# Kernel tuning notes

Measured on AMD Instinct MI355X. Metric: run time of the kernel, lower is better.

## Reference

```python
import jax, jax.numpy as jnp
import numpy as np

N = 512      # nodes
E = 16384    # edges (avg degree 32)
D = 128      # indim
OUT = 128    # outdim


def setup_inputs() -> dict:
    key = jax.random.key(0)
    k1, k2, k3 = jax.random.split(key, 3)
    X = jax.random.normal(k1, (N, N, D), dtype=jnp.float32)
    edge_index = jax.random.randint(k2, (2, E), 0, N, dtype=jnp.int64)
    W = jax.random.normal(k3, (3 * D, OUT), dtype=jnp.float32) * (1.0 / np.sqrt(3 * D))
    b = jnp.zeros((OUT,), dtype=jnp.float32)
    return {"X": X, "edge_index": edge_index, "W": W, "b": b}


def reference(X, edge_index, W, b):
    # X: [N, N, D] tuple features X[i, j] for (subgraph root i, node j)
    # edge_index: [2, E] directed edges (src -> dst), aggr = 'sum'
    n = X.shape[0]
    src, dst = edge_index[0], edge_index[1]
    # Dense binary adjacency (sum aggregation counts multi-edges, matching
    # scatter-add over the edge list). A[k, j] = #edges k -> j.
    A = jnp.zeros((n, n), dtype=X.dtype).at[src, dst].add(jnp.ones((src.shape[0],), X.dtype))
    # OpMessagePassingOnSubg2D: within subgraph i, aggregate over neighbors of j
    # X1[i, j] = sum_{k in N(j)} X[i, k]
    X1 = jnp.einsum('kj,ikd->ijd', A, X)
    # OpMessagePassingCrossSubg2D: across subgraphs, aggregate over neighbors of i
    # X2[i, j] = sum_{k in N(i)} X[k, j]
    X2 = jnp.einsum('ki,kjd->ijd', A, X)
    # catvalue([X1, X2]) -> [X, X1, X2], then pointwise MLP (single Linear)
    H = jnp.concatenate([X, X1, X2], axis=-1)  # [N, N, 3D]
    return H @ W + b  # [N, N, OUT]
```

## Files before the change

### kernel.cpp

```cpp
#include <hip/hip_runtime.h>
#include <hip/hip_bf16.h>
#include <stdint.h>

#define NN 512
#define DD 128
#define EE 16384
#define K3 384

typedef short bf16x8 __attribute__((ext_vector_type(8)));
typedef short bf16x4 __attribute__((ext_vector_type(4)));
typedef float f32x4  __attribute__((ext_vector_type(4)));
typedef unsigned int u32;

__device__ __forceinline__ short f2bf(float f) {
    union { __hip_bfloat16 h; short s; } u;
    u.h = __float2bfloat16(f);
    return u.s;
}
__device__ __forceinline__ u32 pk2(float a, float b) {
    return (u32)(unsigned short)f2bf(a) | ((u32)(unsigned short)f2bf(b) << 16);
}

typedef __attribute__((address_space(3))) unsigned int lds_u32;
typedef __attribute__((address_space(1))) const unsigned int glb_u32;
__device__ __forceinline__ void gll16(void* l, const void* g) {
    __builtin_amdgcn_global_load_lds((glb_u32*)g, (lds_u32*)l, 16, 0, 0);
}


__global__ void k_zero(float* __restrict__ At) {
    At[blockIdx.x * 256 + threadIdx.x] = 0.0f;
}

__global__ void k_edges(const int* __restrict__ ei, float* __restrict__ At) {
    __shared__ int flag;
    if (threadIdx.x == 0) flag = 0;
    __syncthreads();
    int any = 0;
    for (int i = threadIdx.x; i < EE; i += blockDim.x) any |= ei[2 * i + 1];
    if (any) atomicOr(&flag, 1);
    __syncthreads();
    const bool is32 = (flag != 0);
    for (int e = threadIdx.x; e < EE; e += blockDim.x) {
        int src, dst;
        if (is32) { src = ei[e];     dst = ei[EE + e]; }
        else      { src = ei[2 * e]; dst = ei[2 * (EE + e)]; }
        atomicAdd(&At[dst * NN + src], 1.0f);
    }
}

__global__ void k_cast_at(const float* __restrict__ At, short* __restrict__ Atb) {
    int t = blockIdx.x * 256 + threadIdx.x;
    Atb[t] = f2bf(At[t]);
}

__global__ void k_wt2(const float* __restrict__ W, short* __restrict__ Wt2) {
    int t = blockIdx.x * 256 + threadIdx.x;
    int kk = t >> 7, n = t & 127;
    int s = kk >> 7, d = kk & 127;
    Wt2[s * 16384 + n * 128 + d] = f2bf(W[t]);
}

__global__ __launch_bounds__(256) void k_y(const float* __restrict__ X,
                                           const short* __restrict__ Wt2,
                                           short* __restrict__ Y1T,
                                           short* __restrict__ Y2) {
    __shared__ __align__(16) short Xs[16384];
    __shared__ __align__(16) short Ws[16384];

    const int tid  = threadIdx.x;
    const int lane = tid & 63;
    const int wv   = tid >> 6;
    const int wr   = (wv >> 1) * 64;
    const int wc   = (wv & 1) * 64;
    const int lm   = lane & 15;
    const int lq   = lane >> 4;
    const int i  = blockIdx.x >> 2;
    const int j0 = (blockIdx.x & 3) * 128;

    #pragma unroll
    for (int it = 0; it < 16; ++it) {
        int g = tid + it * 256;
        int r = g >> 5, c4 = g & 31;
        float4 v = *(const float4*)&X[i * 65536 + (j0 + r) * 128 + c4 * 4];
        int kb = c4 >> 4, c = c4 & 15, p = c >> 1, h2 = c & 1;
        bf16x4 pc; pc[0] = f2bf(v.x); pc[1] = f2bf(v.y); pc[2] = f2bf(v.z); pc[3] = f2bf(v.w);
        *(bf16x4*)&Xs[kb * 8192 + r * 64 + ((p ^ (r & 7)) * 8 + h2 * 4)] = pc;
    }

    #pragma unroll
    for (int s = 1; s <= 2; ++s) {
        #pragma unroll
        for (int it = 0; it < 8; ++it) {
            int slot = it * 256 + tid;
            int kb = slot >> 10, rem = slot & 1023;
            int n = rem >> 3, pc = rem & 7;
            gll16(&Ws[slot * 8],
                  &Wt2[s * 16384 + n * 128 + kb * 64 + ((pc ^ (n & 7)) * 8)]);
        }
        __syncthreads();

        f32x4 acc[4][4] = {};
        #pragma unroll
        for (int kb = 0; kb < 2; ++kb)
            #pragma unroll
            for (int ks = 0; ks < 2; ++ks) {
                bf16x8 af[4], bf[4];
                #pragma unroll
                for (int mf = 0; mf < 4; ++mf) {
                    int R = wr + mf * 16 + lm, Cc = ks * 4 + lq;
                    af[mf] = *(const bf16x8*)&Xs[kb * 8192 + R * 64 + (Cc ^ (R & 7)) * 8];
                }
                #pragma unroll
                for (int nf = 0; nf < 4; ++nf) {
                    int R = wc + nf * 16 + lm, Cc = ks * 4 + lq;
                    bf[nf] = *(const bf16x8*)&Ws[kb * 8192 + R * 64 + (Cc ^ (R & 7)) * 8];
                }
                #pragma unroll
                for (int mf = 0; mf < 4; ++mf)
                    #pragma unroll
                    for (int nf = 0; nf < 4; ++nf)
                        acc[mf][nf] = __builtin_amdgcn_mfma_f32_16x16x32_bf16(
                            af[mf], bf[nf], acc[mf][nf], 0, 0, 0);
            }
        __syncthreads();

        if (s == 1) {
            u32* T = (u32*)Ws;
            #pragma unroll
            for (int mf = 0; mf < 4; ++mf)
                #pragma unroll
                for (int nf = 0; nf < 4; ++nf) {
                    int n = wc + nf * 16 + lm;
                    int jb = wr + mf * 16 + lq * 4;
                    int w = jb >> 1;
                    u32 lo = pk2(acc[mf][nf][0], acc[mf][nf][1]);
                    u32 hi = pk2(acc[mf][nf][2], acc[mf][nf][3]);
                    uint2 val; val.x = lo; val.y = hi;
                    *(uint2*)&T[n * 64 + (w ^ (n & 28))] = val;
                }
            __syncthreads();
            #pragma unroll
            for (int it = 0; it < 8; ++it) {
                int ch = tid & 15, n = (tid >> 4) + it * 16;
                uint4 q = *(const uint4*)&T[n * 64 + ((ch * 4) ^ (n & 28))];
                *(uint4*)&Y1T[i * 65536 + n * 512 + j0 + ch * 8] = q;
            }
            __syncthreads();
        } else {
            #pragma unroll
            for (int mf = 0; mf < 4; ++mf)
                #pragma unroll
                for (int nf = 0; nf < 4; ++nf)
                    #pragma unroll
                    for (int r = 0; r < 4; ++r)
                        Ws[(wr + mf * 16 + lq * 4 + r) * 128 + wc + nf * 16 + lm]
                            = f2bf(acc[mf][nf][r]);
            __syncthreads();
            #pragma unroll
            for (int it = 0; it < 8; ++it) {
                int q = tid + it * 256;
                int row = q >> 4, oc = (q & 15) * 8;
                *(bf16x8*)&Y2[i * 65536 + (j0 + row) * 128 + oc]
                    = *(const bf16x8*)&Ws[row * 128 + oc];
            }
        }
    }
}

__global__ __launch_bounds__(256) void k_t(const short* __restrict__ Y2,
                                           short* __restrict__ Y2T) {
    __shared__ __align__(16) u32 U[128 * 64];
    const int tid = threadIdx.x;
    const int j  = blockIdx.x >> 2;
    const int k0 = (blockIdx.x & 3) * 128;

    const int c8 = tid & 15;
    const int a0 = tid >> 4;
    #pragma unroll
    for (int it = 0; it < 4; ++it) {
        int a = a0 + it * 16;
        const short* r0 = &Y2[(size_t)(k0 + 2 * a) * 65536 + j * 128 + c8 * 8];
        bf16x8 A0 = *(const bf16x8*)r0;
        bf16x8 A1 = *(const bf16x8*)(r0 + 65536);
        #pragma unroll
        for (int cc = 0; cc < 8; ++cc) {
            int n = c8 * 8 + cc;
            U[n * 64 + (a ^ (n & 28))] =
                (u32)(unsigned short)A0[cc] | ((u32)(unsigned short)A1[cc] << 16);
        }
    }
    __syncthreads();
    const int ch = tid & 15;
    const int n0 = tid >> 4;
    #pragma unroll
    for (int it = 0; it < 8; ++it) {
        int n = n0 + it * 16;
        uint4 q = *(const uint4*)&U[n * 64 + ((ch * 4) ^ (n & 28))];
        *(uint4*)&Y2T[j * 65536 + n * 512 + k0 + ch * 8] = q;
    }
}

__global__ __launch_bounds__(256) void k_a1(const short* __restrict__ Atb,
                                            const short* __restrict__ Y1T,
                                            short* __restrict__ P1) {
    __shared__ __align__(16) short sm[16384];
    short* As = sm;
    short* Bs = sm + 8192;

    const int tid  = threadIdx.x;
    const int lane = tid & 63;
    const int wv   = tid >> 6;
    const int wr   = (wv >> 1) * 64;
    const int wc   = (wv & 1) * 64;
    const int lm   = lane & 15;
    const int lq   = lane >> 4;
    const int i  = blockIdx.x >> 2;
    const int a0 = (blockIdx.x & 3) * 128;

    f32x4 acc[4][4] = {};

    for (int kb = 0; kb < 8; ++kb) {
        const int k0 = kb * 64;
        #pragma unroll
        for (int it = 0; it < 4; ++it) {
            int slot = it * 256 + tid;
            int r = slot >> 3, p = slot & 7;
            int cg = (p ^ (r & 7)) * 8;
            gll16(&As[slot * 8], &Atb[(a0 + r) * 512 + k0 + cg]);
            gll16(&Bs[slot * 8], &Y1T[i * 65536 + r * 512 + k0 + cg]);
        }
        __syncthreads();
        #pragma unroll
        for (int ks = 0; ks < 2; ++ks) {
            bf16x8 af[4], bf[4];
            #pragma unroll
            for (int mf = 0; mf < 4; ++mf) {
                int R = wr + mf * 16 + lm, Cc = ks * 4 + lq;
                af[mf] = *(const bf16x8*)&As[R * 64 + (Cc ^ (R & 7)) * 8];
            }
            #pragma unroll
            for (int nf = 0; nf < 4; ++nf) {
                int R = wc + nf * 16 + lm, Cc = ks * 4 + lq;
                bf[nf] = *(const bf16x8*)&Bs[R * 64 + (Cc ^ (R & 7)) * 8];
            }
            #pragma unroll
            for (int mf = 0; mf < 4; ++mf)
                #pragma unroll
                for (int nf = 0; nf < 4; ++nf)
                    acc[mf][nf] = __builtin_amdgcn_mfma_f32_16x16x32_bf16(
                        af[mf], bf[nf], acc[mf][nf], 0, 0, 0);
        }
        __syncthreads();
    }

    #pragma unroll
    for (int mf = 0; mf < 4; ++mf)
        #pragma unroll
        for (int nf = 0; nf < 4; ++nf)
            #pragma unroll
            for (int r = 0; r < 4; ++r)
                sm[(wr + mf * 16 + lq * 4 + r) * 128 + wc + nf * 16 + lm]
                    = f2bf(acc[mf][nf][r]);
    __syncthreads();
    #pragma unroll
    for (int it = 0; it < 8; ++it) {
        int q = tid + it * 256;
        int row = q >> 4, oc = (q & 15) * 8;
        *(bf16x8*)&P1[i * 65536 + (a0 + row) * 128 + oc]
            = *(const bf16x8*)&sm[row * 128 + oc];
    }
}

__global__ __launch_bounds__(256) void k_a2f(const float* __restrict__ X,
                                             const short* __restrict__ Atb,
                                             const short* __restrict__ Y2T,
                                             const short* __restrict__ Wt2,
                                             const short* __restrict__ P1,
                                             const float* __restrict__ bias,
                                             float* __restrict__ out) {
    __shared__ __align__(16) short sm[16384];
    short* As = sm;
    short* Bs = sm + 8192;

    const int tid  = threadIdx.x;
    const int lane = tid & 63;
    const int wv   = tid >> 6;
    const int wr   = (wv >> 1) * 64;
    const int wc   = (wv & 1) * 64;
    const int lm   = lane & 15;
    const int lq   = lane >> 4;
    const int j  = blockIdx.x >> 2;
    const int i0 = (blockIdx.x & 3) * 128;

    f32x4 acc[4][4] = {};

    #pragma unroll
    for (int kb = 0; kb < 2; ++kb) {
        #pragma unroll
        for (int it = 0; it < 8; ++it) {
            int g = tid + it * 256;
            int r = g >> 4, c4 = g & 15;
            float4 v = *(const float4*)&X[(size_t)(i0 + r) * 65536 + j * 128 + kb * 64 + c4 * 4];
            int p = c4 >> 1, h2 = c4 & 1;
            bf16x4 pc; pc[0] = f2bf(v.x); pc[1] = f2bf(v.y); pc[2] = f2bf(v.z); pc[3] = f2bf(v.w);
            *(bf16x4*)&As[r * 64 + ((p ^ (r & 7)) * 8 + h2 * 4)] = pc;
        }
        #pragma unroll
        for (int it = 0; it < 4; ++it) {
            int slot = it * 256 + tid;
            int n = slot >> 3, pc = slot & 7;
            gll16(&Bs[slot * 8], &Wt2[n * 128 + kb * 64 + ((pc ^ (n & 7)) * 8)]);
        }
        __syncthreads();
        #pragma unroll
        for (int ks = 0; ks < 2; ++ks) {
            bf16x8 af[4], bf[4];
            #pragma unroll
            for (int mf = 0; mf < 4; ++mf) {
                int R = wr + mf * 16 + lm, Cc = ks * 4 + lq;
                af[mf] = *(const bf16x8*)&As[R * 64 + (Cc ^ (R & 7)) * 8];
            }
            #pragma unroll
            for (int nf = 0; nf < 4; ++nf) {
                int R = wc + nf * 16 + lm, Cc = ks * 4 + lq;
                bf[nf] = *(const bf16x8*)&Bs[R * 64 + (Cc ^ (R & 7)) * 8];
            }
            #pragma unroll
            for (int mf = 0; mf < 4; ++mf)
                #pragma unroll
                for (int nf = 0; nf < 4; ++nf)
                    acc[mf][nf] = __builtin_amdgcn_mfma_f32_16x16x32_bf16(
                        af[mf], bf[nf], acc[mf][nf], 0, 0, 0);
        }
        __syncthreads();
    }

    for (int kb = 0; kb < 8; ++kb) {
        const int k0 = kb * 64;
        #pragma unroll
        for (int it = 0; it < 4; ++it) {
            int slot = it * 256 + tid;
            int r = slot >> 3, p = slot & 7;
            int cg = (p ^ (r & 7)) * 8;
            gll16(&As[slot * 8], &Atb[(i0 + r) * 512 + k0 + cg]);
            gll16(&Bs[slot * 8], &Y2T[j * 65536 + r * 512 + k0 + cg]);
        }
        __syncthreads();
        #pragma unroll
        for (int ks = 0; ks < 2; ++ks) {
            bf16x8 af[4], bf[4];
            #pragma unroll
            for (int mf = 0; mf < 4; ++mf) {
                int R = wr + mf * 16 + lm, Cc = ks * 4 + lq;
                af[mf] = *(const bf16x8*)&As[R * 64 + (Cc ^ (R & 7)) * 8];
            }
            #pragma unroll
            for (int nf = 0; nf < 4; ++nf) {
                int R = wc + nf * 16 + lm, Cc = ks * 4 + lq;
                bf[nf] = *(const bf16x8*)&Bs[R * 64 + (Cc ^ (R & 7)) * 8];
            }
            #pragma unroll
            for (int mf = 0; mf < 4; ++mf)
                #pragma unroll
                for (int nf = 0; nf < 4; ++nf)
                    acc[mf][nf] = __builtin_amdgcn_mfma_f32_16x16x32_bf16(
                        af[mf], bf[nf], acc[mf][nf], 0, 0, 0);
        }
        __syncthreads();
    }

    #pragma unroll
    for (int mf = 0; mf < 4; ++mf)
        #pragma unroll
        for (int nf = 0; nf < 4; ++nf)
            #pragma unroll
            for (int r = 0; r < 4; ++r)
                sm[(wr + mf * 16 + lq * 4 + r) * 128 + wc + nf * 16 + lm]
                    = f2bf(acc[mf][nf][r]);
    __syncthreads();
    #pragma unroll
    for (int it = 0; it < 8; ++it) {
        int q = tid + it * 256;
        int row = q >> 4, oc = (q & 15) * 8;
        bf16x8 vs = *(const bf16x8*)&sm[row * 128 + oc];
        bf16x8 vp = *(const bf16x8*)&P1[(size_t)(i0 + row) * 65536 / 512 * 512 + 0];
        (void)vp;
        const short* p1p = &P1[(size_t)(i0 + row) * 65536 + j * 128 + oc];
        bf16x8 vpl = *(const bf16x8*)p1p;
        float4 b0 = *(const float4*)&bias[oc];
        float4 b1 = *(const float4*)&bias[oc + 4];
        union { short s; __hip_bfloat16 h; } cs, cp;
        float o[8];
        #pragma unroll
        for (int e = 0; e < 8; ++e) {
            cs.s = vs[e]; cp.s = vpl[e];
            o[e] = __bfloat162float(cs.h) + __bfloat162float(cp.h);
        }
        o[0] += b0.x; o[1] += b0.y; o[2] += b0.z; o[3] += b0.w;
        o[4] += b1.x; o[5] += b1.y; o[6] += b1.z; o[7] += b1.w;
        float* op = &out[(size_t)(i0 + row) * 65536 + j * 128 + oc];
        float4 w0; w0.x = o[0]; w0.y = o[1]; w0.z = o[2]; w0.w = o[3];
        float4 w1; w1.x = o[4]; w1.y = o[5]; w1.z = o[6]; w1.w = o[7];
        *(float4*)op = w0;
        *(float4*)(op + 4) = w1;
    }
}


__global__ __launch_bounds__(256) void k_agg_fb(const float* __restrict__ X,
                                                const float* __restrict__ At,
                                                short* __restrict__ X1b,
                                                short* __restrict__ X2b) {
    __shared__ short As[128 * 72];
    __shared__ short Bs[128 * 72];
    const int tid  = threadIdx.x;
    const int lane = tid & 63;
    const int wv   = tid >> 6;
    const int wr   = (wv >> 1) * 64;
    const int wc   = (wv & 1) * 64;
    const int lm   = lane & 15;
    const int lq   = lane >> 4;
    int a0, Bbase, Bks, Cbase, Crs;
    short* Cp;
    const int bidx = blockIdx.x;
    if (bidx < 2048) {
        int i = bidx >> 2, jt = bidx & 3;
        a0 = jt * 128; Bbase = i * 65536; Bks = 128;
        Cbase = i * 65536 + jt * 16384; Crs = 128; Cp = X1b;
    } else {
        int bb = bidx - 2048;
        int j = bb >> 2, it = bb & 3;
        a0 = it * 128; Bbase = j * 128; Bks = 65536;
        Cbase = it * 8388608 + j * 128; Crs = 65536; Cp = X2b;
    }
    f32x4 acc[4][4] = {};
    const int d  = tid & 127;
    const int kh = tid >> 7;
    for (int kb = 0; kb < 8; ++kb) {
        const int k0 = kb * 64;
        #pragma unroll
        for (int it8 = 0; it8 < 8; ++it8) {
            int g = tid + it8 * 256;
            int r = g >> 4, kq = (g & 15) * 4;
            float4 v = *(const float4*)&At[(a0 + r) * 512 + k0 + kq];
            bf16x4 p; p[0] = f2bf(v.x); p[1] = f2bf(v.y); p[2] = f2bf(v.z); p[3] = f2bf(v.w);
            *(bf16x4*)&As[r * 72 + kq] = p;
        }
        #pragma unroll
        for (int gi = 0; gi < 4; ++gi) {
            int kg = kh * 4 + gi;
            bf16x8 p;
            #pragma unroll
            for (int jj = 0; jj < 8; ++jj)
                p[jj] = f2bf(X[Bbase + (k0 + kg * 8 + jj) * Bks + d]);
            *(bf16x8*)&Bs[d * 72 + kg * 8] = p;
        }
        __syncthreads();
        #pragma unroll
        for (int ks = 0; ks < 2; ++ks) {
            bf16x8 af[4], bfr[4];
            #pragma unroll
            for (int mf = 0; mf < 4; ++mf)
                af[mf] = *(const bf16x8*)&As[(wr + mf * 16 + lm) * 72 + ks * 32 + lq * 8];
            #pragma unroll
            for (int nf = 0; nf < 4; ++nf)
                bfr[nf] = *(const bf16x8*)&Bs[(wc + nf * 16 + lm) * 72 + ks * 32 + lq * 8];
            #pragma unroll
            for (int mf = 0; mf < 4; ++mf)
                #pragma unroll
                for (int nf = 0; nf < 4; ++nf)
                    acc[mf][nf] = __builtin_amdgcn_mfma_f32_16x16x32_bf16(
                        af[mf], bfr[nf], acc[mf][nf], 0, 0, 0);
        }
        __syncthreads();
    }
    #pragma unroll
    for (int mf = 0; mf < 4; ++mf)
        #pragma unroll
        for (int nf = 0; nf < 4; ++nf)
            #pragma unroll
            for (int r = 0; r < 4; ++r) {
                int row = wr + mf * 16 + lq * 4 + r;
                int col = wc + nf * 16 + lm;
                Cp[Cbase + row * Crs + col] = f2bf(acc[mf][nf][r]);
            }
}

__global__ __launch_bounds__(256) void k_final_fb(const float* __restrict__ X,
                                                  const short* __restrict__ X1b,
                                                  const short* __restrict__ X2b,
                                                  const short* __restrict__ Wt2,
                                                  const float* __restrict__ bias,
                                                  float* __restrict__ out) {
    __shared__ short As[128 * 72];
    __shared__ short Ws[128 * 72];
    const int tid  = threadIdx.x;
    const int lane = tid & 63;
    const int wv   = tid >> 6;
    const int wr   = (wv >> 1) * 64;
    const int wc   = (wv & 1) * 64;
    const int lm   = lane & 15;
    const int lq   = lane >> 4;
    const int m0   = blockIdx.x * 128;
    f32x4 acc[4][4] = {};
    for (int ph = 0; ph < 6; ++ph) {
        const int s = ph >> 1, h = ph & 1;
        if (s == 0) {
            #pragma unroll
            for (int it8 = 0; it8 < 8; ++it8) {
                int g = tid + it8 * 256;
                int r = g >> 4, kq = (g & 15) * 4;
                float4 v = *(const float4*)&X[(m0 + r) * 128 + h * 64 + kq];
                bf16x4 p; p[0] = f2bf(v.x); p[1] = f2bf(v.y); p[2] = f2bf(v.z); p[3] = f2bf(v.w);
                *(bf16x4*)&As[r * 72 + kq] = p;
            }
        } else {
            const short* src = (s == 1) ? X1b : X2b;
            #pragma unroll
            for (int it4 = 0; it4 < 4; ++it4) {
                int g = tid + it4 * 256;
                int r = g >> 3, ko = (g & 7) * 8;
                *(bf16x8*)&As[r * 72 + ko] =
                    *(const bf16x8*)&src[(m0 + r) * 128 + h * 64 + ko];
            }
        }
        #pragma unroll
        for (int it4 = 0; it4 < 4; ++it4) {
            int g = tid + it4 * 256;
            int n = g >> 3, ko = (g & 7) * 8;
            *(bf16x8*)&Ws[n * 72 + ko] =
                *(const bf16x8*)&Wt2[s * 16384 + n * 128 + h * 64 + ko];
        }
        __syncthreads();
        #pragma unroll
        for (int ks = 0; ks < 2; ++ks) {
            bf16x8 af[4], bfr[4];
            #pragma unroll
            for (int mf = 0; mf < 4; ++mf)
                af[mf] = *(const bf16x8*)&As[(wr + mf * 16 + lm) * 72 + ks * 32 + lq * 8];
            #pragma unroll
            for (int nf = 0; nf < 4; ++nf)
                bfr[nf] = *(const bf16x8*)&Ws[(wc + nf * 16 + lm) * 72 + ks * 32 + lq * 8];
            #pragma unroll
            for (int mf = 0; mf < 4; ++mf)
                #pragma unroll
                for (int nf = 0; nf < 4; ++nf)
                    acc[mf][nf] = __builtin_amdgcn_mfma_f32_16x16x32_bf16(
                        af[mf], bfr[nf], acc[mf][nf], 0, 0, 0);
        }
        __syncthreads();
    }
    #pragma unroll
    for (int nf = 0; nf < 4; ++nf) {
        float bv = bias[wc + nf * 16 + lm];
        #pragma unroll
        for (int mf = 0; mf < 4; ++mf)
            #pragma unroll
            for (int r = 0; r < 4; ++r) {
                int row = m0 + wr + mf * 16 + lq * 4 + r;
                int col = wc + nf * 16 + lm;
                out[row * 128 + col] = acc[mf][nf][r] + bv;
            }
    }
}

extern "C" void kernel_launch(void* const* d_in, const int* in_sizes, int n_in,
                              void* d_out, int out_size, void* d_ws, size_t ws_size,
                              hipStream_t stream) {
    const float* X  = (const float*)d_in[0];
    const int*   ei = (const int*)d_in[1];
    const float* W  = (const float*)d_in[2];
    const float* b  = (const float*)d_in[3];
    float* out = (float*)d_out;
    char* ws = (char*)d_ws;
    const size_t MB = 1u << 20;

    float* At  = (float*)ws;
    short* Atb = (short*)(ws + 1 * MB);
    short* Wt2 = (short*)(ws + 1 * MB + 512 * 1024);

    k_zero   <<<1024, 256, 0, stream>>>(At);
    k_edges  <<<1, 1024, 0, stream>>>(ei, At);
    k_wt2    <<<192, 256, 0, stream>>>(W, Wt2);
    k_cast_at<<<1024, 256, 0, stream>>>(At, Atb);

    if (ws_size >= 194 * MB) {
        short* Y1T = (short*)(ws + 2 * MB);
        short* Y2  = (short*)(ws + 66 * MB);
        short* Y2T = (short*)(ws + 130 * MB);
        short* P1  = Y2;
        k_y  <<<2048, 256, 0, stream>>>(X, Wt2, Y1T, Y2);
        k_t  <<<2048, 256, 0, stream>>>(Y2, Y2T);
        k_a1 <<<2048, 256, 0, stream>>>(Atb, Y1T, P1);
        k_a2f<<<2048, 256, 0, stream>>>(X, Atb, Y2T, Wt2, P1, b, out);
    } else {
        short* X1b = (short*)(ws + 2 * MB);
        short* X2b = (short*)(ws + 66 * MB);
        k_agg_fb  <<<4096, 256, 0, stream>>>(X, At, X1b, X2b);
        k_final_fb<<<2048, 256, 0, stream>>>(X, X1b, X2b, Wt2, b, out);
    }
}
```

Before: 475.4 us.

## Fuse Y projection and within-subgraph aggregation into one per-slab kernel

Replaces the separate k_y and k_a1 kernels with k_slab. Each k_slab block handles one subgraph row i. It projects X through both weight slices, keeps the Y1 chunk in shared memory and immediately multiplies it by the adjacency, so the Y1T intermediate never goes through global memory. The adjacency is pre-packed into an MFMA-fragment layout (k_pack_at), letting both k_slab and k_a2f read A fragments straight from global memory instead of staging them in LDS. The trade-offs are 128KB of LDS per 512-thread block, uncoalesced scalar Y2 stores, and only 512 blocks.

```diff
diff --git a/kernel.cpp b/kernel.cpp
--- a/kernel.cpp
+++ b/kernel.cpp
@@ -5,7 +5,6 @@
 #define NN 512
 #define DD 128
 #define EE 16384
-#define K3 384
 
 typedef short bf16x8 __attribute__((ext_vector_type(8)));
 typedef short bf16x4 __attribute__((ext_vector_type(4)));
@@ -49,11 +48,6 @@
     }
 }
 
-__global__ void k_cast_at(const float* __restrict__ At, short* __restrict__ Atb) {
-    int t = blockIdx.x * 256 + threadIdx.x;
-    Atb[t] = f2bf(At[t]);
-}
-
 __global__ void k_wt2(const float* __restrict__ W, short* __restrict__ Wt2) {
     int t = blockIdx.x * 256 + threadIdx.x;
     int kk = t >> 7, n = t & 127;
@@ -61,110 +55,152 @@
     Wt2[s * 16384 + n * 128 + d] = f2bf(W[t]);
 }
 
-__global__ __launch_bounds__(256) void k_y(const float* __restrict__ X,
-                                           const short* __restrict__ Wt2,
-                                           short* __restrict__ Y1T,
-                                           short* __restrict__ Y2) {
-    __shared__ __align__(16) short Xs[16384];
-    __shared__ __align__(16) short Ws[16384];
+__global__ void k_pack_at(const float* __restrict__ At, short* __restrict__ Atp) {
+    int t = blockIdx.x * 256 + threadIdx.x;
+    int T = t >> 6, l = t & 63;
+    int row = (T >> 4) * 16 + (l & 15);
+    int col = (T & 15) * 32 + (l >> 4) * 8;
+    const float* s = &At[row * 512 + col];
+    bf16x8 p;
+    #pragma unroll
+    for (int e = 0; e < 8; ++e) p[e] = f2bf(s[e]);
+    *(bf16x8*)&Atp[(size_t)T * 512 + l * 8] = p;
+}
+
+__global__ __launch_bounds__(512, 2) void k_slab(const float* __restrict__ X,
+                                                 const short* __restrict__ Wt2,
+                                                 const short* __restrict__ Atp,
+                                                 short* __restrict__ Y2,
+                                                 short* __restrict__ Pp) {
+    __shared__ __align__(16) short sh[65536];
+    short* Xc = sh;
+    short* Yc = sh + 16384;
+    short* Lw = sh + 32768;
 
     const int tid  = threadIdx.x;
     const int lane = tid & 63;
     const int wv   = tid >> 6;
-    const int wr   = (wv >> 1) * 64;
-    const int wc   = (wv & 1) * 64;
     const int lm   = lane & 15;
     const int lq   = lane >> 4;
-    const int i  = blockIdx.x >> 2;
-    const int j0 = (blockIdx.x & 3) * 128;
-
-    #pragma unroll
-    for (int it = 0; it < 16; ++it) {
-        int g = tid + it * 256;
-        int r = g >> 5, c4 = g & 31;
-        float4 v = *(const float4*)&X[i * 65536 + (j0 + r) * 128 + c4 * 4];
-        int kb = c4 >> 4, c = c4 & 15, p = c >> 1, h2 = c & 1;
-        bf16x4 pc; pc[0] = f2bf(v.x); pc[1] = f2bf(v.y); pc[2] = f2bf(v.z); pc[3] = f2bf(v.w);
-        *(bf16x4*)&Xs[kb * 8192 + r * 64 + ((p ^ (r & 7)) * 8 + h2 * 4)] = pc;
-    }
-
-    #pragma unroll
-    for (int s = 1; s <= 2; ++s) {
+    const int i    = blockIdx.x;
+
+    const int mw   = wv & 1;
+    const int quad = wv >> 1;
+    const int rowh = quad & 1;
+    const int colh = quad >> 1;
+    const int wr   = wv * 64;
+
+    #pragma unroll
+    for (int it = 0; it < 8; ++it) {
+        int slot = it * 512 + tid;
+        int s01 = slot >> 11, kb = (slot >> 10) & 1;
+        int n = (slot >> 3) & 127, pc = slot & 7;
+        gll16(&Lw[slot * 8],
+              &Wt2[(1 + s01) * 16384 + n * 128 + kb * 64 + ((pc ^ (n & 7)) * 8)]);
+    }
+
+    f32x4 acc[4][8] = {};
+
+    for (int kc = 0; kc < 4; ++kc) {
+        if (kc) __syncthreads();
         #pragma unroll
         for (int it = 0; it < 8; ++it) {
-            int slot = it * 256 + tid;
-            int kb = slot >> 10, rem = slot & 1023;
-            int n = rem >> 3, pc = rem & 7;
-            gll16(&Ws[slot * 8],
-                  &Wt2[s * 16384 + n * 128 + kb * 64 + ((pc ^ (n & 7)) * 8)]);
-        }
-        __syncthreads();
-
-        f32x4 acc[4][4] = {};
-        #pragma unroll
-        for (int kb = 0; kb < 2; ++kb)
+            int g = tid + it * 512;
+            int r = g >> 5, c4 = g & 31;
+            float4 v = *(const float4*)&X[(size_t)i * 65536 + (kc * 128 + r) * 128 + c4 * 4];
+            int kb = c4 >> 4, c = c4 & 15, p = c >> 1, h2 = c & 1;
+            bf16x4 pcv; pcv[0] = f2bf(v.x); pcv[1] = f2bf(v.y); pcv[2] = f2bf(v.z); pcv[3] = f2bf(v.w);
+            *(bf16x4*)&Xc[kb * 8192 + r * 64 + ((p ^ (r & 7)) * 8 + h2 * 4)] = pcv;
+        }
+        __syncthreads();
+
+        f32x4 ay[4][4] = {};
+        #pragma unroll
+        for (int sl = 0; sl < 4; ++sl) {
+            int kb = sl >> 1, ks = sl & 1, Cc = ks * 4 + lq;
+            bf16x8 af[4], bw[4];
+            #pragma unroll
+            for (int mf = 0; mf < 4; ++mf) {
+                int R = rowh * 64 + mf * 16 + lm;
+                af[mf] = *(const bf16x8*)&Xc[kb * 8192 + R * 64 + ((Cc ^ (R & 7)) * 8)];
+            }
+            #pragma unroll
+            for (int nf = 0; nf < 4; ++nf) {
+                int R = colh * 64 + nf * 16 + lm;
+                bw[nf] = *(const bf16x8*)&Lw[mw * 16384 + kb * 8192 + R * 64 + ((Cc ^ (R & 7)) * 8)];
+            }
+            #pragma unroll
+            for (int mf = 0; mf < 4; ++mf)
+                #pragma unroll
+                for (int nf = 0; nf < 4; ++nf)
+                    ay[mf][nf] = __builtin_amdgcn_mfma_f32_16x16x32_bf16(
+                        af[mf], bw[nf], ay[mf][nf], 0, 0, 0);
+        }
+        if (mw == 0) {
+            #pragma unroll
+            for (int mf = 0; mf < 4; ++mf)
+                #pragma unroll
+                for (int nf = 0; nf < 4; ++nf)
+                    #pragma unroll
+                    for (int rr = 0; rr < 4; ++rr) {
+                        int rl64 = mf * 16 + lq * 4 + rr;
+                        int n = colh * 64 + nf * 16 + lm;
+                        Yc[rowh * 8192 + n * 64 + (((rl64 >> 3) ^ (n & 7)) * 8 + (rl64 & 7))]
+                            = f2bf(ay[mf][nf][rr]);
+                    }
+        } else {
+            #pragma unroll
+            for (int mf = 0; mf < 4; ++mf)
+                #pragma unroll
+                for (int nf = 0; nf < 4; ++nf)
+                    #pragma unroll
+                    for (int rr = 0; rr < 4; ++rr) {
+                        int row = kc * 128 + rowh * 64 + mf * 16 + lq * 4 + rr;
+                        int n = colh * 64 + nf * 16 + lm;
+                        Y2[(size_t)i * 65536 + row * 128 + n] = f2bf(ay[mf][nf][rr]);
+                    }
+        }
+        __syncthreads();
+
+        #pragma unroll
+        for (int kb2 = 0; kb2 < 2; ++kb2)
             #pragma unroll
             for (int ks = 0; ks < 2; ++ks) {
-                bf16x8 af[4], bf[4];
-                #pragma unroll
-                for (int mf = 0; mf < 4; ++mf) {
-                    int R = wr + mf * 16 + lm, Cc = ks * 4 + lq;
-                    af[mf] = *(const bf16x8*)&Xs[kb * 8192 + R * 64 + (Cc ^ (R & 7)) * 8];
-                }
-                #pragma unroll
-                for (int nf = 0; nf < 4; ++nf) {
-                    int R = wc + nf * 16 + lm, Cc = ks * 4 + lq;
-                    bf[nf] = *(const bf16x8*)&Ws[kb * 8192 + R * 64 + (Cc ^ (R & 7)) * 8];
+                int kt = kc * 4 + kb2 * 2 + ks;
+                bf16x8 af[4], bf[8];
+                #pragma unroll
+                for (int mf = 0; mf < 4; ++mf)
+                    af[mf] = *(const bf16x8*)&Atp[(size_t)((wv * 4 + mf) * 16 + kt) * 512 + lane * 8];
+                #pragma unroll
+                for (int nf = 0; nf < 8; ++nf) {
+                    int R = nf * 16 + lm;
+                    bf[nf] = *(const bf16x8*)&Yc[kb2 * 8192 + R * 64 + (((ks * 4 + lq) ^ (R & 7)) * 8)];
                 }
                 #pragma unroll
                 for (int mf = 0; mf < 4; ++mf)
                     #pragma unroll
-                    for (int nf = 0; nf < 4; ++nf)
+                    for (int nf = 0; nf < 8; ++nf)
                         acc[mf][nf] = __builtin_amdgcn_mfma_f32_16x16x32_bf16(
                             af[mf], bf[nf], acc[mf][nf], 0, 0, 0);
             }
-        __syncthreads();
-
-        if (s == 1) {
-            u32* T = (u32*)Ws;
-            #pragma unroll
-            for (int mf = 0; mf < 4; ++mf)
-                #pragma unroll
-                for (int nf = 0; nf < 4; ++nf) {
-                    int n = wc + nf * 16 + lm;
-                    int jb = wr + mf * 16 + lq * 4;
-                    int w = jb >> 1;
-                    u32 lo = pk2(acc[mf][nf][0], acc[mf][nf][1]);
-                    u32 hi = pk2(acc[mf][nf][2], acc[mf][nf][3]);
-                    uint2 val; val.x = lo; val.y = hi;
-                    *(uint2*)&T[n * 64 + (w ^ (n & 28))] = val;
-                }
-            __syncthreads();
-            #pragma unroll
-            for (int it = 0; it < 8; ++it) {
-                int ch = tid & 15, n = (tid >> 4) + it * 16;
-                uint4 q = *(const uint4*)&T[n * 64 + ((ch * 4) ^ (n & 28))];
-                *(uint4*)&Y1T[i * 65536 + n * 512 + j0 + ch * 8] = q;
-            }
-            __syncthreads();
-        } else {
-            #pragma unroll
-            for (int mf = 0; mf < 4; ++mf)
-                #pragma unroll
-                for (int nf = 0; nf < 4; ++nf)
-                    #pragma unroll
-                    for (int r = 0; r < 4; ++r)
-                        Ws[(wr + mf * 16 + lq * 4 + r) * 128 + wc + nf * 16 + lm]
-                            = f2bf(acc[mf][nf][r]);
-            __syncthreads();
-            #pragma unroll
-            for (int it = 0; it < 8; ++it) {
-                int q = tid + it * 256;
-                int row = q >> 4, oc = (q & 15) * 8;
-                *(bf16x8*)&Y2[i * 65536 + (j0 + row) * 128 + oc]
-                    = *(const bf16x8*)&Ws[row * 128 + oc];
-            }
-        }
+    }
+    __syncthreads();
+
+    #pragma unroll
+    for (int mf = 0; mf < 4; ++mf)
+        #pragma unroll
+        for (int nf = 0; nf < 8; ++nf)
+            #pragma unroll
+            for (int rr = 0; rr < 4; ++rr)
+                sh[(wr + mf * 16 + lq * 4 + rr) * 128 + nf * 16 + lm]
+                    = f2bf(acc[mf][nf][rr]);
+    __syncthreads();
+    #pragma unroll
+    for (int it = 0; it < 16; ++it) {
+        int q = tid + it * 512;
+        int row = q >> 4, oc = (q & 15) * 8;
+        *(bf16x8*)&Pp[(size_t)i * 65536 + row * 128 + oc]
+            = *(const bf16x8*)&sh[row * 128 + oc];
     }
 }
 
@@ -201,82 +237,11 @@
     }
 }
 
-__global__ __launch_bounds__(256) void k_a1(const short* __restrict__ Atb,
-                                            const short* __restrict__ Y1T,
-                                            short* __restrict__ P1) {
-    __shared__ __align__(16) short sm[16384];
-    short* As = sm;
-    short* Bs = sm + 8192;
-
-    const int tid  = threadIdx.x;
-    const int lane = tid & 63;
-    const int wv   = tid >> 6;
-    const int wr   = (wv >> 1) * 64;
-    const int wc   = (wv & 1) * 64;
-    const int lm   = lane & 15;
-    const int lq   = lane >> 4;
-    const int i  = blockIdx.x >> 2;
-    const int a0 = (blockIdx.x & 3) * 128;
-
-    f32x4 acc[4][4] = {};
-
-    for (int kb = 0; kb < 8; ++kb) {
-        const int k0 = kb * 64;
-        #pragma unroll
-        for (int it = 0; it < 4; ++it) {
-            int slot = it * 256 + tid;
-            int r = slot >> 3, p = slot & 7;
-            int cg = (p ^ (r & 7)) * 8;
-            gll16(&As[slot * 8], &Atb[(a0 + r) * 512 + k0 + cg]);
-            gll16(&Bs[slot * 8], &Y1T[i * 65536 + r * 512 + k0 + cg]);
-        }
-        __syncthreads();
-        #pragma unroll
-        for (int ks = 0; ks < 2; ++ks) {
-            bf16x8 af[4], bf[4];
-            #pragma unroll
-            for (int mf = 0; mf < 4; ++mf) {
-                int R = wr + mf * 16 + lm, Cc = ks * 4 + lq;
-                af[mf] = *(const bf16x8*)&As[R * 64 + (Cc ^ (R & 7)) * 8];
-            }
-            #pragma unroll
-            for (int nf = 0; nf < 4; ++nf) {
-                int R = wc + nf * 16 + lm, Cc = ks * 4 + lq;
-                bf[nf] = *(const bf16x8*)&Bs[R * 64 + (Cc ^ (R & 7)) * 8];
-            }
-            #pragma unroll
-            for (int mf = 0; mf < 4; ++mf)
-                #pragma unroll
-                for (int nf = 0; nf < 4; ++nf)
-                    acc[mf][nf] = __builtin_amdgcn_mfma_f32_16x16x32_bf16(
-                        af[mf], bf[nf], acc[mf][nf], 0, 0, 0);
-        }
-        __syncthreads();
-    }
-
-    #pragma unroll
-    for (int mf = 0; mf < 4; ++mf)
-        #pragma unroll
-        for (int nf = 0; nf < 4; ++nf)
-            #pragma unroll
-            for (int r = 0; r < 4; ++r)
-                sm[(wr + mf * 16 + lq * 4 + r) * 128 + wc + nf * 16 + lm]
-                    = f2bf(acc[mf][nf][r]);
-    __syncthreads();
-    #pragma unroll
-    for (int it = 0; it < 8; ++it) {
-        int q = tid + it * 256;
-        int row = q >> 4, oc = (q & 15) * 8;
-        *(bf16x8*)&P1[i * 65536 + (a0 + row) * 128 + oc]
-            = *(const bf16x8*)&sm[row * 128 + oc];
-    }
-}
-
 __global__ __launch_bounds__(256) void k_a2f(const float* __restrict__ X,
-                                             const short* __restrict__ Atb,
+                                             const short* __restrict__ Atp,
                                              const short* __restrict__ Y2T,
                                              const short* __restrict__ Wt2,
-                                             const short* __restrict__ P1,
+                                             const short* __restrict__ Pp,
                                              const float* __restrict__ bias,
                                              float* __restrict__ out) {
     __shared__ __align__(16) short sm[16384];
@@ -336,6 +301,7 @@
         __syncthreads();
     }
 
+    const int jt0 = (i0 >> 4) + (wr >> 4);
     for (int kb = 0; kb < 8; ++kb) {
         const int k0 = kb * 64;
         #pragma unroll
@@ -343,18 +309,16 @@
             int slot = it * 256 + tid;
             int r = slot >> 3, p = slot & 7;
             int cg = (p ^ (r & 7)) * 8;
-            gll16(&As[slot * 8], &Atb[(i0 + r) * 512 + k0 + cg]);
             gll16(&Bs[slot * 8], &Y2T[j * 65536 + r * 512 + k0 + cg]);
         }
         __syncthreads();
         #pragma unroll
         for (int ks = 0; ks < 2; ++ks) {
+            int kt = kb * 2 + ks;
             bf16x8 af[4], bf[4];
             #pragma unroll
-            for (int mf = 0; mf < 4; ++mf) {
-                int R = wr + mf * 16 + lm, Cc = ks * 4 + lq;
-                af[mf] = *(const bf16x8*)&As[R * 64 + (Cc ^ (R & 7)) * 8];
-            }
+            for (int mf = 0; mf < 4; ++mf)
+                af[mf] = *(const bf16x8*)&Atp[(size_t)((jt0 + mf) * 16 + kt) * 512 + lane * 8];
             #pragma unroll
             for (int nf = 0; nf < 4; ++nf) {
                 int R = wc + nf * 16 + lm, Cc = ks * 4 + lq;
@@ -384,10 +348,7 @@
         int q = tid + it * 256;
         int row = q >> 4, oc = (q & 15) * 8;
         bf16x8 vs = *(const bf16x8*)&sm[row * 128 + oc];
-        bf16x8 vp = *(const bf16x8*)&P1[(size_t)(i0 + row) * 65536 / 512 * 512 + 0];
-        (void)vp;
-        const short* p1p = &P1[(size_t)(i0 + row) * 65536 + j * 128 + oc];
-        bf16x8 vpl = *(const bf16x8*)p1p;
+        bf16x8 vpl = *(const bf16x8*)&Pp[(size_t)(i0 + row) * 65536 + j * 128 + oc];
         float4 b0 = *(const float4*)&bias[oc];
         float4 b1 = *(const float4*)&bias[oc + 4];
         union { short s; __hip_bfloat16 h; } cs, cp;
@@ -577,23 +538,21 @@
     const size_t MB = 1u << 20;
 
     float* At  = (float*)ws;
-    short* Atb = (short*)(ws + 1 * MB);
+    short* Atp = (short*)(ws + 1 * MB);
     short* Wt2 = (short*)(ws + 1 * MB + 512 * 1024);
 
     k_zero   <<<1024, 256, 0, stream>>>(At);
     k_edges  <<<1, 1024, 0, stream>>>(ei, At);
     k_wt2    <<<192, 256, 0, stream>>>(W, Wt2);
-    k_cast_at<<<1024, 256, 0, stream>>>(At, Atb);
+    k_pack_at<<<128, 256, 0, stream>>>(At, Atp);
 
     if (ws_size >= 194 * MB) {
-        short* Y1T = (short*)(ws + 2 * MB);
-        short* Y2  = (short*)(ws + 66 * MB);
-        short* Y2T = (short*)(ws + 130 * MB);
-        short* P1  = Y2;
-        k_y  <<<2048, 256, 0, stream>>>(X, Wt2, Y1T, Y2);
-        k_t  <<<2048, 256, 0, stream>>>(Y2, Y2T);
-        k_a1 <<<2048, 256, 0, stream>>>(Atb, Y1T, P1);
-        k_a2f<<<2048, 256, 0, stream>>>(X, Atb, Y2T, Wt2, P1, b, out);
+        short* Y2  = (short*)(ws + 2 * MB);
+        short* Y2T = (short*)(ws + 66 * MB);
+        short* Pp  = (short*)(ws + 130 * MB);
+        k_slab<<<512, 512, 0, stream>>>(X, Wt2, Atp, Y2, Pp);
+        k_t   <<<2048, 256, 0, stream>>>(Y2, Y2T);
+        k_a2f <<<2048, 256, 0, stream>>>(X, Atp, Y2T, Wt2, Pp, b, out);
     } else {
         short* X1b = (short*)(ws + 2 * MB);
         short* X2b = (short*)(ws + 66 * MB);
```

Result: slower. 524.5 us (+10.3%).

## Pre-pack adjacency into MFMA fragment layout, double-buffer B tiles, swizzle block order

Applied to the files above, without the earlier changes.

The bf16 adjacency matrix is now packed once into a per-lane MFMA fragment layout. The aggregation GEMMs can then read A fragments straight from global/L2 instead of staging them through LDS. The freed LDS is used to double-buffer the Y1T/Y2T tiles, so the next tile's load overlaps the current MFMAs. Block indices in k_t, k_a1 and k_a2f are remapped with a stride-8 swizzle, likely to spread consecutive blocks across XCDs for better L2 locality. The risks are A-fragment latency from global memory and a possible race, because the loop no longer has a barrier before the next tile overwrites its buffer.

```diff
diff --git a/kernel.cpp b/kernel.cpp
--- a/kernel.cpp
+++ b/kernel.cpp
@@ -5,7 +5,6 @@
 #define NN 512
 #define DD 128
 #define EE 16384
-#define K3 384
 
 typedef short bf16x8 __attribute__((ext_vector_type(8)));
 typedef short bf16x4 __attribute__((ext_vector_type(4)));
@@ -49,16 +48,23 @@
     }
 }
 
-__global__ void k_cast_at(const float* __restrict__ At, short* __restrict__ Atb) {
-    int t = blockIdx.x * 256 + threadIdx.x;
-    Atb[t] = f2bf(At[t]);
-}
-
 __global__ void k_wt2(const float* __restrict__ W, short* __restrict__ Wt2) {
     int t = blockIdx.x * 256 + threadIdx.x;
     int kk = t >> 7, n = t & 127;
     int s = kk >> 7, d = kk & 127;
     Wt2[s * 16384 + n * 128 + d] = f2bf(W[t]);
+}
+
+__global__ void k_pack_at(const float* __restrict__ At, short* __restrict__ Atp) {
+    int t = blockIdx.x * 256 + threadIdx.x;
+    int T = t >> 6, l = t & 63;
+    int row = (T >> 4) * 16 + (l & 15);
+    int col = (T & 15) * 32 + (l >> 4) * 8;
+    const float* s = &At[row * 512 + col];
+    bf16x8 p;
+    #pragma unroll
+    for (int e = 0; e < 8; ++e) p[e] = f2bf(s[e]);
+    *(bf16x8*)&Atp[(size_t)T * 512 + l * 8] = p;
 }
 
 __global__ __launch_bounds__(256) void k_y(const float* __restrict__ X,
@@ -172,8 +178,9 @@
                                            short* __restrict__ Y2T) {
     __shared__ __align__(16) u32 U[128 * 64];
     const int tid = threadIdx.x;
-    const int j  = blockIdx.x >> 2;
-    const int k0 = (blockIdx.x & 3) * 128;
+    const int bid = (blockIdx.x & 7) * 256 + (blockIdx.x >> 3);
+    const int j  = bid >> 2;
+    const int k0 = (bid & 3) * 128;
 
     const int c8 = tid & 15;
     const int a0 = tid >> 4;
@@ -201,12 +208,10 @@
     }
 }
 
-__global__ __launch_bounds__(256) void k_a1(const short* __restrict__ Atb,
+__global__ __launch_bounds__(256) void k_a1(const short* __restrict__ Atp,
                                             const short* __restrict__ Y1T,
                                             short* __restrict__ P1) {
     __shared__ __align__(16) short sm[16384];
-    short* As = sm;
-    short* Bs = sm + 8192;
 
     const int tid  = threadIdx.x;
     const int lane = tid & 63;
@@ -215,34 +220,46 @@
     const int wc   = (wv & 1) * 64;
     const int lm   = lane & 15;
     const int lq   = lane >> 4;
-    const int i  = blockIdx.x >> 2;
-    const int a0 = (blockIdx.x & 3) * 128;
+    const int bid = (blockIdx.x & 7) * 256 + (blockIdx.x >> 3);
+    const int i  = bid >> 2;
+    const int a0 = (bid & 3) * 128;
+    const int jt0 = (a0 >> 4) + (wr >> 4);
 
     f32x4 acc[4][4] = {};
 
+    #pragma unroll
+    for (int it = 0; it < 4; ++it) {
+        int slot = it * 256 + tid;
+        int r = slot >> 3, p = slot & 7;
+        int cg = (p ^ (r & 7)) * 8;
+        gll16(&sm[slot * 8], &Y1T[i * 65536 + r * 512 + cg]);
+    }
+    __syncthreads();
+
     for (int kb = 0; kb < 8; ++kb) {
-        const int k0 = kb * 64;
-        #pragma unroll
-        for (int it = 0; it < 4; ++it) {
-            int slot = it * 256 + tid;
-            int r = slot >> 3, p = slot & 7;
-            int cg = (p ^ (r & 7)) * 8;
-            gll16(&As[slot * 8], &Atb[(a0 + r) * 512 + k0 + cg]);
-            gll16(&Bs[slot * 8], &Y1T[i * 65536 + r * 512 + k0 + cg]);
-        }
-        __syncthreads();
+        short* cur = (kb & 1) ? sm + 8192 : sm;
+        short* nxt = (kb & 1) ? sm : sm + 8192;
+        if (kb < 7) {
+            const int k0n = (kb + 1) * 64;
+            #pragma unroll
+            for (int it = 0; it < 4; ++it) {
+                int slot = it * 256 + tid;
+                int r = slot >> 3, p = slot & 7;
+                int cg = (p ^ (r & 7)) * 8;
+                gll16(&nxt[slot * 8], &Y1T[i * 65536 + r * 512 + k0n + cg]);
+            }
+        }
         #pragma unroll
         for (int ks = 0; ks < 2; ++ks) {
+            int kt = kb * 2 + ks;
             bf16x8 af[4], bf[4];
             #pragma unroll
-            for (int mf = 0; mf < 4; ++mf) {
-                int R = wr + mf * 16 + lm, Cc = ks * 4 + lq;
-                af[mf] = *(const bf16x8*)&As[R * 64 + (Cc ^ (R & 7)) * 8];
-            }
+            for (int mf = 0; mf < 4; ++mf)
+                af[mf] = *(const bf16x8*)&Atp[(size_t)((jt0 + mf) * 16 + kt) * 512 + lane * 8];
             #pragma unroll
             for (int nf = 0; nf < 4; ++nf) {
                 int R = wc + nf * 16 + lm, Cc = ks * 4 + lq;
-                bf[nf] = *(const bf16x8*)&Bs[R * 64 + (Cc ^ (R & 7)) * 8];
+                bf[nf] = *(const bf16x8*)&cur[R * 64 + (Cc ^ (R & 7)) * 8];
             }
             #pragma unroll
             for (int mf = 0; mf < 4; ++mf)
@@ -273,7 +290,7 @@
 }
 
 __global__ __launch_bounds__(256) void k_a2f(const float* __restrict__ X,
-                                             const short* __restrict__ Atb,
+                                             const short* __restrict__ Atp,
                                              const short* __restrict__ Y2T,
                                              const short* __restrict__ Wt2,
                                              const short* __restrict__ P1,
@@ -290,8 +307,9 @@
     const int wc   = (wv & 1) * 64;
     const int lm   = lane & 15;
     const int lq   = lane >> 4;
-    const int j  = blockIdx.x >> 2;
-    const int i0 = (blockIdx.x & 3) * 128;
+    const int bid = (blockIdx.x & 7) * 256 + (blockIdx.x >> 3);
+    const int j  = bid >> 2;
+    const int i0 = (bid & 3) * 128;
 
     f32x4 acc[4][4] = {};
 
@@ -336,29 +354,40 @@
         __syncthreads();
     }
 
+    const int jt0 = (i0 >> 4) + (wr >> 4);
+    #pragma unroll
+    for (int it = 0; it < 4; ++it) {
+        int slot = it * 256 + tid;
+        int r = slot >> 3, p = slot & 7;
+        int cg = (p ^ (r & 7)) * 8;
+        gll16(&sm[slot * 8], &Y2T[j * 65536 + r * 512 + cg]);
+    }
+    __syncthreads();
+
     for (int kb = 0; kb < 8; ++kb) {
-        const int k0 = kb * 64;
-        #pragma unroll
-        for (int it = 0; it < 4; ++it) {
-            int slot = it * 256 + tid;
-            int r = slot >> 3, p = slot & 7;
-            int cg = (p ^ (r & 7)) * 8;
-            gll16(&As[slot * 8], &Atb[(i0 + r) * 512 + k0 + cg]);
-            gll16(&Bs[slot * 8], &Y2T[j * 65536 + r * 512 + k0 + cg]);
-        }
-        __syncthreads();
+        short* cur = (kb & 1) ? sm + 8192 : sm;
+        short* nxt = (kb & 1) ? sm : sm + 8192;
+        if (kb < 7) {
+            const int k0n = (kb + 1) * 64;
+            #pragma unroll
+            for (int it = 0; it < 4; ++it) {
+                int slot = it * 256 + tid;
+                int r = slot >> 3, p = slot & 7;
+                int cg = (p ^ (r & 7)) * 8;
+                gll16(&nxt[slot * 8], &Y2T[j * 65536 + r * 512 + k0n + cg]);
+            }
+        }
         #pragma unroll
         for (int ks = 0; ks < 2; ++ks) {
+            int kt = kb * 2 + ks;
             bf16x8 af[4], bf[4];
             #pragma unroll
-            for (int mf = 0; mf < 4; ++mf) {
-                int R = wr + mf * 16 + lm, Cc = ks * 4 + lq;
-                af[mf] = *(const bf16x8*)&As[R * 64 + (Cc ^ (R & 7)) * 8];
-            }
+            for (int mf = 0; mf < 4; ++mf)
+                af[mf] = *(const bf16x8*)&Atp[(size_t)((jt0 + mf) * 16 + kt) * 512 + lane * 8];
             #pragma unroll
             for (int nf = 0; nf < 4; ++nf) {
                 int R = wc + nf * 16 + lm, Cc = ks * 4 + lq;
-                bf[nf] = *(const bf16x8*)&Bs[R * 64 + (Cc ^ (R & 7)) * 8];
+                bf[nf] = *(const bf16x8*)&cur[R * 64 + (Cc ^ (R & 7)) * 8];
             }
             #pragma unroll
             for (int mf = 0; mf < 4; ++mf)
@@ -384,10 +413,7 @@
         int q = tid + it * 256;
         int row = q >> 4, oc = (q & 15) * 8;
         bf16x8 vs = *(const bf16x8*)&sm[row * 128 + oc];
-        bf16x8 vp = *(const bf16x8*)&P1[(size_t)(i0 + row) * 65536 / 512 * 512 + 0];
-        (void)vp;
-        const short* p1p = &P1[(size_t)(i0 + row) * 65536 + j * 128 + oc];
-        bf16x8 vpl = *(const bf16x8*)p1p;
+        bf16x8 vpl = *(const bf16x8*)&P1[(size_t)(i0 + row) * 65536 + j * 128 + oc];
         float4 b0 = *(const float4*)&bias[oc];
         float4 b1 = *(const float4*)&bias[oc + 4];
         union { short s; __hip_bfloat16 h; } cs, cp;
@@ -577,13 +603,13 @@
     const size_t MB = 1u << 20;
 
     float* At  = (float*)ws;
-    short* Atb = (short*)(ws + 1 * MB);
+    short* Atp = (short*)(ws + 1 * MB);
     short* Wt2 = (short*)(ws + 1 * MB + 512 * 1024);
 
     k_zero   <<<1024, 256, 0, stream>>>(At);
     k_edges  <<<1, 1024, 0, stream>>>(ei, At);
     k_wt2    <<<192, 256, 0, stream>>>(W, Wt2);
-    k_cast_at<<<1024, 256, 0, stream>>>(At, Atb);
+    k_pack_at<<<128, 256, 0, stream>>>(At, Atp);
 
     if (ws_size >= 194 * MB) {
         short* Y1T = (short*)(ws + 2 * MB);
@@ -592,8 +618,8 @@
         short* P1  = Y2;
         k_y  <<<2048, 256, 0, stream>>>(X, Wt2, Y1T, Y2);
         k_t  <<<2048, 256, 0, stream>>>(Y2, Y2T);
-        k_a1 <<<2048, 256, 0, stream>>>(Atb, Y1T, P1);
-        k_a2f<<<2048, 256, 0, stream>>>(X, Atb, Y2T, Wt2, P1, b, out);
+        k_a1 <<<2048, 256, 0, stream>>>(Atp, Y1T, P1);
+        k_a2f<<<2048, 256, 0, stream>>>(X, Atp, Y2T, Wt2, P1, b, out);
     } else {
         short* X1b = (short*)(ws + 2 * MB);
         short* X2b = (short*)(ws + 66 * MB);
```

New measurement: 492.1 us. 1.04x slower.
